# Optimization experiments

Measured on AMD Instinct MI355X. Metric: run time of the kernel, lower is better.

Reference implementation:

```python
import jax, jax.numpy as jnp
import numpy as np

NUM_EXPERTS = 8
HIDDEN = 1024
INTERMEDIATE = 2816
TOTAL_TOKENS = 4096  # 512 tokens per expert


def setup_inputs() -> dict:
    key = jax.random.key(0)
    k_x, k1, k2, k3 = jax.random.split(key, 4)
    hiddens = jax.random.normal(k_x, (TOTAL_TOKENS, HIDDEN), dtype=jnp.float32)
    # tokens assumed pre-sorted by expert; equal-sized groups here
    batch_sizes = jnp.full((NUM_EXPERTS,), TOTAL_TOKENS // NUM_EXPERTS, dtype=jnp.int64)
    w1_weight = jax.random.normal(k1, (NUM_EXPERTS, HIDDEN, INTERMEDIATE), dtype=jnp.float32)
    w2_weight = jax.random.normal(k2, (NUM_EXPERTS, INTERMEDIATE, HIDDEN), dtype=jnp.float32)
    w3_weight = jax.random.normal(k3, (NUM_EXPERTS, HIDDEN, INTERMEDIATE), dtype=jnp.float32)
    return {
        "hiddens": hiddens,
        "w1_weight": w1_weight,
        "w2_weight": w2_weight,
        "w3_weight": w3_weight,
        "batch_sizes": batch_sizes,
    }


def _grouped_moe(hiddens, w1, w2, w3, batch_sizes):
    """Grouped SwiGLU FFN: tokens are contiguous per expert (sizes = batch_sizes).

    Jit-safe formulation: map each token to its expert id, then run one masked
    dense GEMM trio per expert (small fixed expert count). Zero rows contribute
    exactly zero (silu(0)*0 == 0), so no final masking of the output is needed.
    """
    num_experts = w1.shape[0]
    total_tokens = hiddens.shape[0]
    bounds = jnp.cumsum(batch_sizes)  # [E] exclusive-right boundaries
    expert_ids = jnp.searchsorted(bounds, jnp.arange(total_tokens), side="right")  # [T]
    out = jnp.zeros((total_tokens, w2.shape[-1]), dtype=hiddens.dtype)
    for e in range(num_experts):
        mask = (expert_ids == e)[:, None]  # [T, 1]
        xe = jnp.where(mask, hiddens, 0)   # zero out other experts' tokens
        up = jax.nn.silu(xe @ w1[e]) * (xe @ w3[e])  # [T, F] SwiGLU
        out = out + up @ w2[e]             # [T, H]
    return out


def reference(hiddens, w1_weight, w2_weight, w3_weight, batch_sizes):
    return _grouped_moe(hiddens, w1_weight, w2_weight, w3_weight, batch_sizes)
```

## Files before the change

kernel.cpp:

```cpp
#include <hip/hip_runtime.h>
#include <hip/hip_bf16.h>

#define NE 8
#define HD 1024
#define ID 2816
#define TT 4096
#define BM 128
#define BK 32
#define BN1 64
#define BN2 64
#define MAXMT (TT / BM + NE)
#define NKS1 (HD / BK)
#define NKS2 (ID / BK)
#define ATILE 8192

typedef __attribute__((ext_vector_type(4))) float f32x4;
typedef __attribute__((ext_vector_type(8))) short s16x8;
typedef __attribute__((ext_vector_type(4))) int i32x4;

__device__ __forceinline__ unsigned int f2bfpk(float lo, float hi) {
  float2 t; t.x = lo; t.y = hi;
  union { __hip_bfloat162 h2; unsigned int u; } cv;
  cv.h2 = __float22bfloat162_rn(t);
  return cv.u;
}

__device__ __forceinline__ void lds_barrier() {
  asm volatile("s_waitcnt lgkmcnt(0)" ::: "memory");
  __builtin_amdgcn_s_barrier();
}

__device__ __forceinline__ void glds16(const void* g, void* l) {
  __builtin_amdgcn_global_load_lds(
      (const __attribute__((address_space(1))) void*)g,
      (__attribute__((address_space(3))) void*)l, 16, 0, 0);
}

__device__ __forceinline__ bool map_tile(const void* bsp, int mt, int& e,
                                         int& mstart, int& rowend) {
  const int* w = (const int*)bsp;
  bool is64 = (w[1] == 0) && (w[3] == 0) && (w[5] == 0) && (w[7] == 0) &&
              ((w[0] | w[2] | w[4] | w[6]) != 0);
  long long start = 0;
  int rem = mt;
  for (int i = 0; i < NE; ++i) {
    long long b = is64 ? ((const long long*)bsp)[i] : (long long)w[i];
    if (b < 0) b = 0;
    int tiles = (int)((b + BM - 1) / BM);
    if (rem < tiles) {
      long long m0 = start + (long long)rem * BM;
      long long me = start + b;
      if (m0 >= TT) return false;
      if (me > TT) me = TT;
      e = i; mstart = (int)m0; rowend = (int)me;
      return true;
    }
    rem -= tiles;
    start += b;
  }
  return false;
}

__global__ __launch_bounds__(256) void cvt_xt(const float* __restrict__ x,
                                              const void* __restrict__ bsp,
                                              unsigned short* __restrict__ xt) {
  int mt = blockIdx.x >> 5;
  int ks = blockIdx.x & 31;
  int e, mstart, rowend;
  if (!map_tile(bsp, mt, e, mstart, rowend)) return;
  int t = threadIdx.x;
  int lane = t & 63;
  int r = lane & 15, q = lane >> 4;
  unsigned short* ob = xt + ((size_t)mt * NKS1 + ks) * (ATILE / 2);
#pragma unroll
  for (int h = 0; h < 2; ++h) {
    int f = h * 4 + (t >> 6);
    int row = mstart + f * 16 + r;
    s16x8 o = (s16x8)0;
    if (row < rowend) {
      const float* src = x + (size_t)row * HD + ks * 32 + q * 8;
      f32x4 v0 = *(const f32x4*)src;
      f32x4 v1 = *(const f32x4*)(src + 4);
      unsigned int d0 = f2bfpk(v0[0], v0[1]), d1 = f2bfpk(v0[2], v0[3]);
      unsigned int d2 = f2bfpk(v1[0], v1[1]), d3 = f2bfpk(v1[2], v1[3]);
      o[0] = (short)d0; o[1] = (short)(d0 >> 16);
      o[2] = (short)d1; o[3] = (short)(d1 >> 16);
      o[4] = (short)d2; o[5] = (short)(d2 >> 16);
      o[6] = (short)d3; o[7] = (short)(d3 >> 16);
    }
    *(s16x8*)(ob + h * 2048 + t * 8) = o;
  }
}

__global__ __launch_bounds__(256, 3) void moe_gemm1(
    const unsigned short* __restrict__ xt, const float* __restrict__ w1,
    const float* __restrict__ w3, const void* __restrict__ bsp,
    __hip_bfloat16* __restrict__ up) {
  __shared__ __align__(16) char As[4][ATILE];
  __shared__ __align__(16) char B1s[2][4096];
  __shared__ __align__(16) char B3s[2][4096];

  const int NWG = (ID / BN1) * MAXMT;
  int bid = blockIdx.x;
  int logical = (bid & 7) * (NWG >> 3) + (bid >> 3);
  int mt = logical % MAXMT;
  int nt = logical / MAXMT;
  int e, mstart, rowend;
  if (!map_tile(bsp, mt, e, mstart, rowend)) return;
  const int n0 = nt * BN1;
  const int tid = threadIdx.x;
  const int lane = tid & 63;
  const int wv = tid >> 6;
  const int wr = wv >> 1, wc = wv & 1;
  const int q = lane >> 4, r16 = lane & 15;

  const int b_n = tid & 63, b_kq = tid >> 6;
  const int boff = (b_n >> 4) * 1024 + b_kq * 256 + (b_n & 15) * 16;
  const char* agp = (const char*)xt + (size_t)mt * NKS1 * ATILE + tid * 16;
  const float* w1c = w1 + (size_t)e * HD * ID + (size_t)(8 * b_kq) * ID + n0 + b_n;
  const float* w3c = w3 + (size_t)e * HD * ID + (size_t)(8 * b_kq) * ID + n0 + b_n;

  f32x4 acc1[4][2], acc3[4][2];
#pragma unroll
  for (int i = 0; i < 4; ++i)
#pragma unroll
    for (int j = 0; j < 2; ++j) { acc1[i][j] = (f32x4)0.f; acc3[i][j] = (f32x4)0.f; }

  float Wa1[8], Wa3[8], Wb1[8], Wb3[8];

  auto gldsA = [&](int k, int buf) {
    const char* s = agp + (size_t)k * ATILE;
    char* d = &As[buf][0] + tid * 16;
    glds16(s, d);
    glds16(s + 4096, d + 4096);
  };
  auto loadB = [&](float* W1_, float* W3_) {
#pragma unroll
    for (int i = 0; i < 8; ++i) {
      W1_[i] = w1c[(size_t)i * ID];
      W3_[i] = w3c[(size_t)i * ID];
    }
    w1c += (size_t)BK * ID; w3c += (size_t)BK * ID;
  };
  auto storeB = [&](int buf, const float* W1_, const float* W3_) {
    i32x4 p1, p3;
    p1[0] = (int)f2bfpk(W1_[0], W1_[1]); p1[1] = (int)f2bfpk(W1_[2], W1_[3]);
    p1[2] = (int)f2bfpk(W1_[4], W1_[5]); p1[3] = (int)f2bfpk(W1_[6], W1_[7]);
    *(i32x4*)(B1s[buf] + boff) = p1;
    p3[0] = (int)f2bfpk(W3_[0], W3_[1]); p3[1] = (int)f2bfpk(W3_[2], W3_[3]);
    p3[2] = (int)f2bfpk(W3_[4], W3_[5]); p3[3] = (int)f2bfpk(W3_[6], W3_[7]);
    *(i32x4*)(B3s[buf] + boff) = p3;
  };
  auto compute = [&](int ab, int bb) {
    s16x8 a[4], b1[2], b3[2];
#pragma unroll
    for (int i = 0; i < 4; ++i)
      a[i] = *(const s16x8*)(As[ab] + (wr * 4 + i) * 1024 + lane * 16);
#pragma unroll
    for (int j = 0; j < 2; ++j) {
      b1[j] = *(const s16x8*)(B1s[bb] + (wc * 2 + j) * 1024 + lane * 16);
      b3[j] = *(const s16x8*)(B3s[bb] + (wc * 2 + j) * 1024 + lane * 16);
    }
#pragma unroll
    for (int i = 0; i < 4; ++i)
#pragma unroll
      for (int j = 0; j < 2; ++j) {
        acc1[i][j] = __builtin_amdgcn_mfma_f32_16x16x32_bf16(a[i], b1[j], acc1[i][j], 0, 0, 0);
        acc3[i][j] = __builtin_amdgcn_mfma_f32_16x16x32_bf16(a[i], b3[j], acc3[i][j], 0, 0, 0);
      }
  };

#define G1PHASE(AB, GD, BB, SB, LW1, LW3, SW1, SW3, KC)    \
  if (kt + (KC) + 2 < NKS1) {                              \
    gldsA(kt + (KC) + 2, (GD));                            \
    __builtin_amdgcn_sched_barrier(0);                     \
    loadB(LW1, LW3);                                       \
  }                                                        \
  compute((AB), (BB));                                     \
  if (kt + (KC) + 1 < NKS1) {                              \
    storeB((SB), SW1, SW3);                                \
    lds_barrier();                                         \
  }

  gldsA(0, 0); gldsA(1, 1);
  __builtin_amdgcn_sched_barrier(0);
  loadB(Wa1, Wa3);
  loadB(Wb1, Wb3);
  storeB(0, Wa1, Wa3);
  lds_barrier();

  for (int kt = 0; kt < NKS1; kt += 4) {
    G1PHASE(0, 2, 0, 1, Wa1, Wa3, Wb1, Wb3, 0)
    G1PHASE(1, 3, 1, 0, Wb1, Wb3, Wa1, Wa3, 1)
    G1PHASE(2, 0, 0, 1, Wa1, Wa3, Wb1, Wb3, 2)
    G1PHASE(3, 1, 1, 0, Wb1, Wb3, Wa1, Wa3, 3)
  }
#undef G1PHASE

#pragma unroll
  for (int i = 0; i < 4; ++i)
#pragma unroll
    for (int r = 0; r < 4; ++r) {
      int gm = mstart + wr * 64 + i * 16 + q * 4 + r;
      if (gm < rowend) {
#pragma unroll
        for (int j = 0; j < 2; ++j) {
          float v1 = acc1[i][j][r], v3 = acc3[i][j][r];
          float s = v1 / (1.f + __expf(-v1));
          up[(size_t)gm * ID + n0 + wc * 32 + j * 16 + r16] = __float2bfloat16(s * v3);
        }
      }
    }
}

__global__ __launch_bounds__(256, 3) void moe_gemm2(
    const __hip_bfloat16* __restrict__ up, const float* __restrict__ w2,
    const void* __restrict__ bsp, float* __restrict__ out) {
  __shared__ __align__(16) char As[2][BM * 80];
  __shared__ __align__(16) char Bs[2][4096];

  const int NWG = (HD / BN2) * MAXMT;
  int bid = blockIdx.x;
  int logical = (bid & 7) * (NWG >> 3) + (bid >> 3);
  int mt = logical % MAXMT;
  int nt = logical / MAXMT;
  int e, mstart, rowend;
  if (!map_tile(bsp, mt, e, mstart, rowend)) return;
  const int n0 = nt * BN2;
  const int tid = threadIdx.x;
  const int lane = tid & 63;
  const int wv = tid >> 6;
  const int wr = wv >> 1, wc = wv & 1;
  const int q = lane >> 4, r16 = lane & 15;

  const int a_k8 = (tid & 3) * 8;
  const int a_r0 = tid >> 2;
  const int b_n = tid & 63, b_kq = tid >> 6;
  const int boff = (b_n >> 4) * 1024 + b_kq * 256 + (b_n & 15) * 16;

  const bool ok0 = (mstart + a_r0) < rowend;
  const bool ok1 = (mstart + a_r0 + 64) < rowend;

  const __hip_bfloat16* uc = up + (size_t)(mstart + a_r0) * ID + a_k8;
  const float* w2c = w2 + (size_t)e * ID * HD + (size_t)(8 * b_kq) * HD + n0 + b_n;

  f32x4 acc[4][2];
#pragma unroll
  for (int i = 0; i < 4; ++i)
#pragma unroll
    for (int j = 0; j < 2; ++j) acc[i][j] = (f32x4)0.f;

  s16x8 Aa[2], Ab[2];
  float Wa[8], Wb[8];

  auto loadT = [&](s16x8* A, float* W_) {
    A[0] = ok0 ? *(const s16x8*)uc : (s16x8)0;
    A[1] = ok1 ? *(const s16x8*)(uc + (size_t)64 * ID) : (s16x8)0;
    uc += BK;
#pragma unroll
    for (int i = 0; i < 8; ++i) W_[i] = w2c[(size_t)i * HD];
    w2c += (size_t)BK * HD;
  };
  auto storeT = [&](int buf, const s16x8* A, const float* W_) {
    *(s16x8*)(As[buf] + a_r0 * 80 + a_k8 * 2) = A[0];
    *(s16x8*)(As[buf] + (a_r0 + 64) * 80 + a_k8 * 2) = A[1];
    i32x4 p;
    p[0] = (int)f2bfpk(W_[0], W_[1]); p[1] = (int)f2bfpk(W_[2], W_[3]);
    p[2] = (int)f2bfpk(W_[4], W_[5]); p[3] = (int)f2bfpk(W_[6], W_[7]);
    *(i32x4*)(Bs[buf] + boff) = p;
  };
  auto compute = [&](int buf) {
    s16x8 a[4], b[2];
#pragma unroll
    for (int i = 0; i < 4; ++i)
      a[i] = *(const s16x8*)(As[buf] + (wr * 64 + i * 16 + r16) * 80 + q * 16);
#pragma unroll
    for (int j = 0; j < 2; ++j)
      b[j] = *(const s16x8*)(Bs[buf] + (wc * 2 + j) * 1024 + lane * 16);
#pragma unroll
    for (int i = 0; i < 4; ++i)
#pragma unroll
      for (int j = 0; j < 2; ++j)
        acc[i][j] = __builtin_amdgcn_mfma_f32_16x16x32_bf16(a[i], b[j], acc[i][j], 0, 0, 0);
  };

#define G2PHASE(AB, SB, LA, LW, SA, SW, KC)                 \
  if (kt + (KC) + 2 < NKS2) { loadT(LA, LW); }              \
  compute(AB);                                              \
  if (kt + (KC) + 1 < NKS2) { storeT((SB), SA, SW); lds_barrier(); }

  loadT(Aa, Wa);
  loadT(Ab, Wb);
  storeT(0, Aa, Wa);
  lds_barrier();
  for (int kt = 0; kt < NKS2; kt += 2) {
    G2PHASE(0, 1, Aa, Wa, Ab, Wb, 0)
    G2PHASE(1, 0, Ab, Wb, Aa, Wa, 1)
  }
#undef G2PHASE

#pragma unroll
  for (int i = 0; i < 4; ++i)
#pragma unroll
    for (int r = 0; r < 4; ++r) {
      int gm = mstart + wr * 64 + i * 16 + q * 4 + r;
      if (gm < rowend) {
#pragma unroll
        for (int j = 0; j < 2; ++j)
          out[(size_t)gm * HD + n0 + wc * 32 + j * 16 + r16] = acc[i][j][r];
      }
    }
}

extern "C" void kernel_launch(void* const* d_in, const int* in_sizes, int n_in,
                              void* d_out, int out_size, void* d_ws, size_t ws_size,
                              hipStream_t stream) {
  const float* x = (const float*)d_in[0];
  const float* w1 = (const float*)d_in[1];
  const float* w2 = (const float*)d_in[2];
  const float* w3 = (const float*)d_in[3];
  const void* bs = d_in[4];
  float* out = (float*)d_out;
  unsigned short* xt = (unsigned short*)d_ws;
  __hip_bfloat16* up =
      (__hip_bfloat16*)((char*)d_ws + (size_t)MAXMT * NKS1 * ATILE);

  hipMemsetAsync(d_out, 0, (size_t)out_size * sizeof(float), stream);

  cvt_xt<<<dim3(MAXMT * NKS1), dim3(256), 0, stream>>>(x, bs, xt);
  moe_gemm1<<<dim3((ID / BN1) * MAXMT), dim3(256), 0, stream>>>(xt, w1, w3, bs, up);
  moe_gemm2<<<dim3((HD / BN2) * MAXMT), dim3(256), 0, stream>>>(up, w2, bs, out);
}
```

Baseline: 184.9 us.

## Load A operands straight from global into registers, bypassing LDS in both GEMMs

Both GEMMs now read the bf16 A operand straight from global memory into MFMA-fragment registers, and A tiles no longer pass through shared memory. The tiled X pre-layout kernel is replaced by a plain row-major fp32-to-bf16 conversion. The aim is to cut LDS traffic and LDS footprint, and gemm2 raises its occupancy hint from 3 to 4. In exchange, each lane issues 16-byte strided global loads across rows, which coalesce worse and rely on L2 hits. Rows past the group boundary read clamped addresses but are masked at store time.

```diff
diff --git a/kernel.cpp b/kernel.cpp
--- a/kernel.cpp
+++ b/kernel.cpp
@@ -12,7 +12,6 @@
 #define MAXMT (TT / BM + NE)
 #define NKS1 (HD / BK)
 #define NKS2 (ID / BK)
-#define ATILE 8192
 
 typedef __attribute__((ext_vector_type(4))) float f32x4;
 typedef __attribute__((ext_vector_type(8))) short s16x8;
@@ -28,12 +27,6 @@
 __device__ __forceinline__ void lds_barrier() {
   asm volatile("s_waitcnt lgkmcnt(0)" ::: "memory");
   __builtin_amdgcn_s_barrier();
-}
-
-__device__ __forceinline__ void glds16(const void* g, void* l) {
-  __builtin_amdgcn_global_load_lds(
-      (const __attribute__((address_space(1))) void*)g,
-      (__attribute__((address_space(3))) void*)l, 16, 0, 0);
 }
 
 __device__ __forceinline__ bool map_tile(const void* bsp, int mt, int& e,
@@ -61,42 +54,25 @@
   return false;
 }
 
-__global__ __launch_bounds__(256) void cvt_xt(const float* __restrict__ x,
-                                              const void* __restrict__ bsp,
-                                              unsigned short* __restrict__ xt) {
-  int mt = blockIdx.x >> 5;
-  int ks = blockIdx.x & 31;
-  int e, mstart, rowend;
-  if (!map_tile(bsp, mt, e, mstart, rowend)) return;
-  int t = threadIdx.x;
-  int lane = t & 63;
-  int r = lane & 15, q = lane >> 4;
-  unsigned short* ob = xt + ((size_t)mt * NKS1 + ks) * (ATILE / 2);
-#pragma unroll
-  for (int h = 0; h < 2; ++h) {
-    int f = h * 4 + (t >> 6);
-    int row = mstart + f * 16 + r;
-    s16x8 o = (s16x8)0;
-    if (row < rowend) {
-      const float* src = x + (size_t)row * HD + ks * 32 + q * 8;
-      f32x4 v0 = *(const f32x4*)src;
-      f32x4 v1 = *(const f32x4*)(src + 4);
-      unsigned int d0 = f2bfpk(v0[0], v0[1]), d1 = f2bfpk(v0[2], v0[3]);
-      unsigned int d2 = f2bfpk(v1[0], v1[1]), d3 = f2bfpk(v1[2], v1[3]);
-      o[0] = (short)d0; o[1] = (short)(d0 >> 16);
-      o[2] = (short)d1; o[3] = (short)(d1 >> 16);
-      o[4] = (short)d2; o[5] = (short)(d2 >> 16);
-      o[6] = (short)d3; o[7] = (short)(d3 >> 16);
-    }
-    *(s16x8*)(ob + h * 2048 + t * 8) = o;
-  }
+__global__ __launch_bounds__(256) void cvt_x(const float* __restrict__ x,
+                                             __hip_bfloat16* __restrict__ xb) {
+  size_t i = ((size_t)blockIdx.x * 256 + threadIdx.x) * 8;
+  f32x4 v0 = *(const f32x4*)(x + i);
+  f32x4 v1 = *(const f32x4*)(x + i + 4);
+  s16x8 o;
+  unsigned int p0 = f2bfpk(v0[0], v0[1]), p1 = f2bfpk(v0[2], v0[3]);
+  unsigned int p2 = f2bfpk(v1[0], v1[1]), p3 = f2bfpk(v1[2], v1[3]);
+  o[0] = (short)(p0 & 0xffff); o[1] = (short)(p0 >> 16);
+  o[2] = (short)(p1 & 0xffff); o[3] = (short)(p1 >> 16);
+  o[4] = (short)(p2 & 0xffff); o[5] = (short)(p2 >> 16);
+  o[6] = (short)(p3 & 0xffff); o[7] = (short)(p3 >> 16);
+  *(s16x8*)((unsigned short*)xb + i) = o;
 }
 
 __global__ __launch_bounds__(256, 3) void moe_gemm1(
-    const unsigned short* __restrict__ xt, const float* __restrict__ w1,
+    const __hip_bfloat16* __restrict__ xbf, const float* __restrict__ w1,
     const float* __restrict__ w3, const void* __restrict__ bsp,
     __hip_bfloat16* __restrict__ up) {
-  __shared__ __align__(16) char As[4][ATILE];
   __shared__ __align__(16) char B1s[2][4096];
   __shared__ __align__(16) char B3s[2][4096];
 
@@ -116,23 +92,42 @@
 
   const int b_n = tid & 63, b_kq = tid >> 6;
   const int boff = (b_n >> 4) * 1024 + b_kq * 256 + (b_n & 15) * 16;
-  const char* agp = (const char*)xt + (size_t)mt * NKS1 * ATILE + tid * 16;
   const float* w1c = w1 + (size_t)e * HD * ID + (size_t)(8 * b_kq) * ID + n0 + b_n;
   const float* w3c = w3 + (size_t)e * HD * ID + (size_t)(8 * b_kq) * ID + n0 + b_n;
 
+  const unsigned short* pA0;
+  const unsigned short* pA1;
+  const unsigned short* pA2;
+  const unsigned short* pA3;
+  {
+    const unsigned short* xb = (const unsigned short*)xbf;
+    int r0 = mstart + wr * 64 + r16;
+    int rowA[4];
+#pragma unroll
+    for (int i = 0; i < 4; ++i) {
+      int r = r0 + i * 16;
+      rowA[i] = r < TT ? r : TT - 1;
+    }
+    pA0 = xb + (size_t)rowA[0] * HD + q * 8;
+    pA1 = xb + (size_t)rowA[1] * HD + q * 8;
+    pA2 = xb + (size_t)rowA[2] * HD + q * 8;
+    pA3 = xb + (size_t)rowA[3] * HD + q * 8;
+  }
+
   f32x4 acc1[4][2], acc3[4][2];
 #pragma unroll
   for (int i = 0; i < 4; ++i)
 #pragma unroll
     for (int j = 0; j < 2; ++j) { acc1[i][j] = (f32x4)0.f; acc3[i][j] = (f32x4)0.f; }
 
+  s16x8 Aa[4], Ab[4];
   float Wa1[8], Wa3[8], Wb1[8], Wb3[8];
 
-  auto gldsA = [&](int k, int buf) {
-    const char* s = agp + (size_t)k * ATILE;
-    char* d = &As[buf][0] + tid * 16;
-    glds16(s, d);
-    glds16(s + 4096, d + 4096);
+  auto loadA = [&](s16x8* A, int k) {
+    A[0] = *(const s16x8*)(pA0 + k * BK);
+    A[1] = *(const s16x8*)(pA1 + k * BK);
+    A[2] = *(const s16x8*)(pA2 + k * BK);
+    A[3] = *(const s16x8*)(pA3 + k * BK);
   };
   auto loadB = [&](float* W1_, float* W3_) {
 #pragma unroll
@@ -151,11 +146,8 @@
     p3[2] = (int)f2bfpk(W3_[4], W3_[5]); p3[3] = (int)f2bfpk(W3_[6], W3_[7]);
     *(i32x4*)(B3s[buf] + boff) = p3;
   };
-  auto compute = [&](int ab, int bb) {
-    s16x8 a[4], b1[2], b3[2];
-#pragma unroll
-    for (int i = 0; i < 4; ++i)
-      a[i] = *(const s16x8*)(As[ab] + (wr * 4 + i) * 1024 + lane * 16);
+  auto compute = [&](const s16x8* A, int bb) {
+    s16x8 b1[2], b3[2];
 #pragma unroll
     for (int j = 0; j < 2; ++j) {
       b1[j] = *(const s16x8*)(B1s[bb] + (wc * 2 + j) * 1024 + lane * 16);
@@ -165,37 +157,26 @@
     for (int i = 0; i < 4; ++i)
 #pragma unroll
       for (int j = 0; j < 2; ++j) {
-        acc1[i][j] = __builtin_amdgcn_mfma_f32_16x16x32_bf16(a[i], b1[j], acc1[i][j], 0, 0, 0);
-        acc3[i][j] = __builtin_amdgcn_mfma_f32_16x16x32_bf16(a[i], b3[j], acc3[i][j], 0, 0, 0);
+        acc1[i][j] = __builtin_amdgcn_mfma_f32_16x16x32_bf16(A[i], b1[j], acc1[i][j], 0, 0, 0);
+        acc3[i][j] = __builtin_amdgcn_mfma_f32_16x16x32_bf16(A[i], b3[j], acc3[i][j], 0, 0, 0);
       }
   };
 
-#define G1PHASE(AB, GD, BB, SB, LW1, LW3, SW1, SW3, KC)    \
-  if (kt + (KC) + 2 < NKS1) {                              \
-    gldsA(kt + (KC) + 2, (GD));                            \
-    __builtin_amdgcn_sched_barrier(0);                     \
-    loadB(LW1, LW3);                                       \
-  }                                                        \
-  compute((AB), (BB));                                     \
-  if (kt + (KC) + 1 < NKS1) {                              \
-    storeB((SB), SW1, SW3);                                \
-    lds_barrier();                                         \
-  }
-
-  gldsA(0, 0); gldsA(1, 1);
-  __builtin_amdgcn_sched_barrier(0);
+  loadA(Aa, 0); loadA(Ab, 1);
   loadB(Wa1, Wa3);
   loadB(Wb1, Wb3);
   storeB(0, Wa1, Wa3);
   lds_barrier();
-
-  for (int kt = 0; kt < NKS1; kt += 4) {
-    G1PHASE(0, 2, 0, 1, Wa1, Wa3, Wb1, Wb3, 0)
-    G1PHASE(1, 3, 1, 0, Wb1, Wb3, Wa1, Wa3, 1)
-    G1PHASE(2, 0, 0, 1, Wa1, Wa3, Wb1, Wb3, 2)
-    G1PHASE(3, 1, 1, 0, Wb1, Wb3, Wa1, Wa3, 3)
-  }
-#undef G1PHASE
+  for (int kt = 0; kt < NKS1; kt += 2) {
+    if (kt + 2 < NKS1) loadB(Wa1, Wa3);
+    compute(Aa, 0);
+    if (kt + 2 < NKS1) loadA(Aa, kt + 2);
+    if (kt + 1 < NKS1) { storeB(1, Wb1, Wb3); lds_barrier(); }
+    if (kt + 3 < NKS1) loadB(Wb1, Wb3);
+    compute(Ab, 1);
+    if (kt + 3 < NKS1) loadA(Ab, kt + 3);
+    if (kt + 2 < NKS1) { storeB(0, Wa1, Wa3); lds_barrier(); }
+  }
 
 #pragma unroll
   for (int i = 0; i < 4; ++i)
@@ -213,10 +194,9 @@
     }
 }
 
-__global__ __launch_bounds__(256, 3) void moe_gemm2(
+__global__ __launch_bounds__(256, 4) void moe_gemm2(
     const __hip_bfloat16* __restrict__ up, const float* __restrict__ w2,
     const void* __restrict__ bsp, float* __restrict__ out) {
-  __shared__ __align__(16) char As[2][BM * 80];
   __shared__ __align__(16) char Bs[2][4096];
 
   const int NWG = (HD / BN2) * MAXMT;
@@ -233,71 +213,82 @@
   const int wr = wv >> 1, wc = wv & 1;
   const int q = lane >> 4, r16 = lane & 15;
 
-  const int a_k8 = (tid & 3) * 8;
-  const int a_r0 = tid >> 2;
   const int b_n = tid & 63, b_kq = tid >> 6;
   const int boff = (b_n >> 4) * 1024 + b_kq * 256 + (b_n & 15) * 16;
-
-  const bool ok0 = (mstart + a_r0) < rowend;
-  const bool ok1 = (mstart + a_r0 + 64) < rowend;
-
-  const __hip_bfloat16* uc = up + (size_t)(mstart + a_r0) * ID + a_k8;
   const float* w2c = w2 + (size_t)e * ID * HD + (size_t)(8 * b_kq) * HD + n0 + b_n;
 
+  const unsigned short* pA0;
+  const unsigned short* pA1;
+  const unsigned short* pA2;
+  const unsigned short* pA3;
+  {
+    const unsigned short* ub = (const unsigned short*)up;
+    int r0 = mstart + wr * 64 + r16;
+    int rowA[4];
+#pragma unroll
+    for (int i = 0; i < 4; ++i) {
+      int r = r0 + i * 16;
+      rowA[i] = r < TT ? r : TT - 1;
+    }
+    pA0 = ub + (size_t)rowA[0] * ID + q * 8;
+    pA1 = ub + (size_t)rowA[1] * ID + q * 8;
+    pA2 = ub + (size_t)rowA[2] * ID + q * 8;
+    pA3 = ub + (size_t)rowA[3] * ID + q * 8;
+  }
+
   f32x4 acc[4][2];
 #pragma unroll
   for (int i = 0; i < 4; ++i)
 #pragma unroll
     for (int j = 0; j < 2; ++j) acc[i][j] = (f32x4)0.f;
 
-  s16x8 Aa[2], Ab[2];
+  s16x8 Aa[4], Ab[4];
   float Wa[8], Wb[8];
 
-  auto loadT = [&](s16x8* A, float* W_) {
-    A[0] = ok0 ? *(const s16x8*)uc : (s16x8)0;
-    A[1] = ok1 ? *(const s16x8*)(uc + (size_t)64 * ID) : (s16x8)0;
-    uc += BK;
+  auto loadA = [&](s16x8* A, int k) {
+    A[0] = *(const s16x8*)(pA0 + k * BK);
+    A[1] = *(const s16x8*)(pA1 + k * BK);
+    A[2] = *(const s16x8*)(pA2 + k * BK);
+    A[3] = *(const s16x8*)(pA3 + k * BK);
+  };
+  auto loadB = [&](float* W_) {
 #pragma unroll
     for (int i = 0; i < 8; ++i) W_[i] = w2c[(size_t)i * HD];
     w2c += (size_t)BK * HD;
   };
-  auto storeT = [&](int buf, const s16x8* A, const float* W_) {
-    *(s16x8*)(As[buf] + a_r0 * 80 + a_k8 * 2) = A[0];
-    *(s16x8*)(As[buf] + (a_r0 + 64) * 80 + a_k8 * 2) = A[1];
+  auto storeB = [&](int buf, const float* W_) {
     i32x4 p;
     p[0] = (int)f2bfpk(W_[0], W_[1]); p[1] = (int)f2bfpk(W_[2], W_[3]);
     p[2] = (int)f2bfpk(W_[4], W_[5]); p[3] = (int)f2bfpk(W_[6], W_[7]);
     *(i32x4*)(Bs[buf] + boff) = p;
   };
-  auto compute = [&](int buf) {
-    s16x8 a[4], b[2];
+  auto compute = [&](const s16x8* A, int bb) {
+    s16x8 b[2];
+#pragma unroll
+    for (int j = 0; j < 2; ++j)
+      b[j] = *(const s16x8*)(Bs[bb] + (wc * 2 + j) * 1024 + lane * 16);
 #pragma unroll
     for (int i = 0; i < 4; ++i)
-      a[i] = *(const s16x8*)(As[buf] + (wr * 64 + i * 16 + r16) * 80 + q * 16);
-#pragma unroll
-    for (int j = 0; j < 2; ++j)
-      b[j] = *(const s16x8*)(Bs[buf] + (wc * 2 + j) * 1024 + lane * 16);
-#pragma unroll
-    for (int i = 0; i < 4; ++i)
 #pragma unroll
       for (int j = 0; j < 2; ++j)
-        acc[i][j] = __builtin_amdgcn_mfma_f32_16x16x32_bf16(a[i], b[j], acc[i][j], 0, 0, 0);
-  };
-
-#define G2PHASE(AB, SB, LA, LW, SA, SW, KC)                 \
-  if (kt + (KC) + 2 < NKS2) { loadT(LA, LW); }              \
-  compute(AB);                                              \
-  if (kt + (KC) + 1 < NKS2) { storeT((SB), SA, SW); lds_barrier(); }
-
-  loadT(Aa, Wa);
-  loadT(Ab, Wb);
-  storeT(0, Aa, Wa);
+        acc[i][j] = __builtin_amdgcn_mfma_f32_16x16x32_bf16(A[i], b[j], acc[i][j], 0, 0, 0);
+  };
+
+  loadA(Aa, 0); loadA(Ab, 1);
+  loadB(Wa);
+  loadB(Wb);
+  storeB(0, Wa);
   lds_barrier();
   for (int kt = 0; kt < NKS2; kt += 2) {
-    G2PHASE(0, 1, Aa, Wa, Ab, Wb, 0)
-    G2PHASE(1, 0, Ab, Wb, Aa, Wa, 1)
-  }
-#undef G2PHASE
+    if (kt + 2 < NKS2) loadB(Wa);
+    compute(Aa, 0);
+    if (kt + 2 < NKS2) loadA(Aa, kt + 2);
+    if (kt + 1 < NKS2) { storeB(1, Wb); lds_barrier(); }
+    if (kt + 3 < NKS2) loadB(Wb);
+    compute(Ab, 1);
+    if (kt + 3 < NKS2) loadA(Ab, kt + 3);
+    if (kt + 2 < NKS2) { storeB(0, Wa); lds_barrier(); }
+  }
 
 #pragma unroll
   for (int i = 0; i < 4; ++i)
@@ -321,13 +312,12 @@
   const float* w3 = (const float*)d_in[3];
   const void* bs = d_in[4];
   float* out = (float*)d_out;
-  unsigned short* xt = (unsigned short*)d_ws;
-  __hip_bfloat16* up =
-      (__hip_bfloat16*)((char*)d_ws + (size_t)MAXMT * NKS1 * ATILE);
+  __hip_bfloat16* xbf = (__hip_bfloat16*)d_ws;
+  __hip_bfloat16* up = (__hip_bfloat16*)((char*)d_ws + (size_t)TT * HD * 2);
 
   hipMemsetAsync(d_out, 0, (size_t)out_size * sizeof(float), stream);
 
-  cvt_xt<<<dim3(MAXMT * NKS1), dim3(256), 0, stream>>>(x, bs, xt);
-  moe_gemm1<<<dim3((ID / BN1) * MAXMT), dim3(256), 0, stream>>>(xt, w1, w3, bs, up);
+  cvt_x<<<dim3(TT * HD / (8 * 256)), dim3(256), 0, stream>>>(x, xbf);
+  moe_gemm1<<<dim3((ID / BN1) * MAXMT), dim3(256), 0, stream>>>(xbf, w1, w3, bs, up);
   moe_gemm2<<<dim3((HD / BN2) * MAXMT), dim3(256), 0, stream>>>(up, w2, bs, out);
 }
```

New measurement: 290.1 us. 1.57x slower.

## Shrink pipeline depth to raise occupancy and use direct-to-LDS loads in gemm2

Applied to the files above, without the earlier changes.

Both GEMM kernels now request 4 workgroups per CU instead of 3. The first GEMM's A-tile LDS ring drops from four buffers to two, and the register double-buffering of weights is cut to a single staging set. The second GEMM stops staging the bf16 intermediate through registers and loads it with global-to-LDS copies into an MFMA-fragment layout, clamping out-of-range rows instead of zeroing them. The aim is lower register and LDS pressure for more resident waves, at the cost of a shallower prefetch window that may expose global-load latency.

```diff
diff --git a/kernel.cpp b/kernel.cpp
--- a/kernel.cpp
+++ b/kernel.cpp
@@ -92,11 +92,11 @@
   }
 }
 
-__global__ __launch_bounds__(256, 3) void moe_gemm1(
+__global__ __launch_bounds__(256, 4) void moe_gemm1(
     const unsigned short* __restrict__ xt, const float* __restrict__ w1,
     const float* __restrict__ w3, const void* __restrict__ bsp,
     __hip_bfloat16* __restrict__ up) {
-  __shared__ __align__(16) char As[4][ATILE];
+  __shared__ __align__(16) char As[2][ATILE];
   __shared__ __align__(16) char B1s[2][4096];
   __shared__ __align__(16) char B3s[2][4096];
 
@@ -126,7 +126,7 @@
 #pragma unroll
     for (int j = 0; j < 2; ++j) { acc1[i][j] = (f32x4)0.f; acc3[i][j] = (f32x4)0.f; }
 
-  float Wa1[8], Wa3[8], Wb1[8], Wb3[8];
+  float Wc1[8], Wc3[8];
 
   auto gldsA = [&](int k, int buf) {
     const char* s = agp + (size_t)k * ATILE;
@@ -134,21 +134,21 @@
     glds16(s, d);
     glds16(s + 4096, d + 4096);
   };
-  auto loadB = [&](float* W1_, float* W3_) {
+  auto loadB = [&]() {
 #pragma unroll
     for (int i = 0; i < 8; ++i) {
-      W1_[i] = w1c[(size_t)i * ID];
-      W3_[i] = w3c[(size_t)i * ID];
+      Wc1[i] = w1c[(size_t)i * ID];
+      Wc3[i] = w3c[(size_t)i * ID];
     }
     w1c += (size_t)BK * ID; w3c += (size_t)BK * ID;
   };
-  auto storeB = [&](int buf, const float* W1_, const float* W3_) {
+  auto storeB = [&](int buf) {
     i32x4 p1, p3;
-    p1[0] = (int)f2bfpk(W1_[0], W1_[1]); p1[1] = (int)f2bfpk(W1_[2], W1_[3]);
-    p1[2] = (int)f2bfpk(W1_[4], W1_[5]); p1[3] = (int)f2bfpk(W1_[6], W1_[7]);
+    p1[0] = (int)f2bfpk(Wc1[0], Wc1[1]); p1[1] = (int)f2bfpk(Wc1[2], Wc1[3]);
+    p1[2] = (int)f2bfpk(Wc1[4], Wc1[5]); p1[3] = (int)f2bfpk(Wc1[6], Wc1[7]);
     *(i32x4*)(B1s[buf] + boff) = p1;
-    p3[0] = (int)f2bfpk(W3_[0], W3_[1]); p3[1] = (int)f2bfpk(W3_[2], W3_[3]);
-    p3[2] = (int)f2bfpk(W3_[4], W3_[5]); p3[3] = (int)f2bfpk(W3_[6], W3_[7]);
+    p3[0] = (int)f2bfpk(Wc3[0], Wc3[1]); p3[1] = (int)f2bfpk(Wc3[2], Wc3[3]);
+    p3[2] = (int)f2bfpk(Wc3[4], Wc3[5]); p3[3] = (int)f2bfpk(Wc3[6], Wc3[7]);
     *(i32x4*)(B3s[buf] + boff) = p3;
   };
   auto compute = [&](int ab, int bb) {
@@ -170,32 +170,29 @@
       }
   };
 
-#define G1PHASE(AB, GD, BB, SB, LW1, LW3, SW1, SW3, KC)    \
-  if (kt + (KC) + 2 < NKS1) {                              \
-    gldsA(kt + (KC) + 2, (GD));                            \
-    __builtin_amdgcn_sched_barrier(0);                     \
-    loadB(LW1, LW3);                                       \
-  }                                                        \
-  compute((AB), (BB));                                     \
-  if (kt + (KC) + 1 < NKS1) {                              \
-    storeB((SB), SW1, SW3);                                \
-    lds_barrier();                                         \
+  gldsA(0, 0);
+  __builtin_amdgcn_sched_barrier(0);
+  loadB();
+  storeB(0);
+  lds_barrier();
+  for (int kt = 0; kt < NKS1; kt += 2) {
+    if (kt + 1 < NKS1) {
+      gldsA(kt + 1, 1);
+      __builtin_amdgcn_sched_barrier(0);
+      loadB();
+      __builtin_amdgcn_sched_barrier(0);
+    }
+    compute(0, 0);
+    if (kt + 1 < NKS1) { storeB(1); lds_barrier(); }
+    if (kt + 2 < NKS1) {
+      gldsA(kt + 2, 0);
+      __builtin_amdgcn_sched_barrier(0);
+      loadB();
+      __builtin_amdgcn_sched_barrier(0);
+    }
+    compute(1, 1);
+    if (kt + 2 < NKS1) { storeB(0); lds_barrier(); }
   }
-
-  gldsA(0, 0); gldsA(1, 1);
-  __builtin_amdgcn_sched_barrier(0);
-  loadB(Wa1, Wa3);
-  loadB(Wb1, Wb3);
-  storeB(0, Wa1, Wa3);
-  lds_barrier();
-
-  for (int kt = 0; kt < NKS1; kt += 4) {
-    G1PHASE(0, 2, 0, 1, Wa1, Wa3, Wb1, Wb3, 0)
-    G1PHASE(1, 3, 1, 0, Wb1, Wb3, Wa1, Wa3, 1)
-    G1PHASE(2, 0, 0, 1, Wa1, Wa3, Wb1, Wb3, 2)
-    G1PHASE(3, 1, 1, 0, Wb1, Wb3, Wa1, Wa3, 3)
-  }
-#undef G1PHASE
 
 #pragma unroll
   for (int i = 0; i < 4; ++i)
@@ -213,10 +210,10 @@
     }
 }
 
-__global__ __launch_bounds__(256, 3) void moe_gemm2(
+__global__ __launch_bounds__(256, 4) void moe_gemm2(
     const __hip_bfloat16* __restrict__ up, const float* __restrict__ w2,
     const void* __restrict__ bsp, float* __restrict__ out) {
-  __shared__ __align__(16) char As[2][BM * 80];
+  __shared__ __align__(16) char As[2][ATILE];
   __shared__ __align__(16) char Bs[2][4096];
 
   const int NWG = (HD / BN2) * MAXMT;
@@ -233,50 +230,50 @@
   const int wr = wv >> 1, wc = wv & 1;
   const int q = lane >> 4, r16 = lane & 15;
 
-  const int a_k8 = (tid & 3) * 8;
-  const int a_r0 = tid >> 2;
   const int b_n = tid & 63, b_kq = tid >> 6;
   const int boff = (b_n >> 4) * 1024 + b_kq * 256 + (b_n & 15) * 16;
-
-  const bool ok0 = (mstart + a_r0) < rowend;
-  const bool ok1 = (mstart + a_r0 + 64) < rowend;
-
-  const __hip_bfloat16* uc = up + (size_t)(mstart + a_r0) * ID + a_k8;
   const float* w2c = w2 + (size_t)e * ID * HD + (size_t)(8 * b_kq) * HD + n0 + b_n;
 
+  int row0 = mstart + (tid >> 6) * 16 + (tid & 15);
+  int row1 = row0 + 64;
+  row0 = row0 < TT ? row0 : TT - 1;
+  row1 = row1 < TT ? row1 : TT - 1;
+  const char* uc0 = (const char*)up + ((size_t)row0 * ID + q * 8) * 2;
+  const char* uc1 = (const char*)up + ((size_t)row1 * ID + q * 8) * 2;
+
   f32x4 acc[4][2];
 #pragma unroll
   for (int i = 0; i < 4; ++i)
 #pragma unroll
     for (int j = 0; j < 2; ++j) acc[i][j] = (f32x4)0.f;
 
-  s16x8 Aa[2], Ab[2];
-  float Wa[8], Wb[8];
-
-  auto loadT = [&](s16x8* A, float* W_) {
-    A[0] = ok0 ? *(const s16x8*)uc : (s16x8)0;
-    A[1] = ok1 ? *(const s16x8*)(uc + (size_t)64 * ID) : (s16x8)0;
-    uc += BK;
-#pragma unroll
-    for (int i = 0; i < 8; ++i) W_[i] = w2c[(size_t)i * HD];
+  float Wc[8];
+
+  auto gldsA = [&](int buf) {
+    char* d = &As[buf][0] + tid * 16;
+    glds16(uc0, d);
+    glds16(uc1, d + 4096);
+    uc0 += BK * 2; uc1 += BK * 2;
+  };
+  auto loadB = [&]() {
+#pragma unroll
+    for (int i = 0; i < 8; ++i) Wc[i] = w2c[(size_t)i * HD];
     w2c += (size_t)BK * HD;
   };
-  auto storeT = [&](int buf, const s16x8* A, const float* W_) {
-    *(s16x8*)(As[buf] + a_r0 * 80 + a_k8 * 2) = A[0];
-    *(s16x8*)(As[buf] + (a_r0 + 64) * 80 + a_k8 * 2) = A[1];
+  auto storeB = [&](int buf) {
     i32x4 p;
-    p[0] = (int)f2bfpk(W_[0], W_[1]); p[1] = (int)f2bfpk(W_[2], W_[3]);
-    p[2] = (int)f2bfpk(W_[4], W_[5]); p[3] = (int)f2bfpk(W_[6], W_[7]);
+    p[0] = (int)f2bfpk(Wc[0], Wc[1]); p[1] = (int)f2bfpk(Wc[2], Wc[3]);
+    p[2] = (int)f2bfpk(Wc[4], Wc[5]); p[3] = (int)f2bfpk(Wc[6], Wc[7]);
     *(i32x4*)(Bs[buf] + boff) = p;
   };
-  auto compute = [&](int buf) {
+  auto compute = [&](int ab, int bb) {
     s16x8 a[4], b[2];
 #pragma unroll
     for (int i = 0; i < 4; ++i)
-      a[i] = *(const s16x8*)(As[buf] + (wr * 64 + i * 16 + r16) * 80 + q * 16);
+      a[i] = *(const s16x8*)(As[ab] + (wr * 4 + i) * 1024 + lane * 16);
 #pragma unroll
     for (int j = 0; j < 2; ++j)
-      b[j] = *(const s16x8*)(Bs[buf] + (wc * 2 + j) * 1024 + lane * 16);
+      b[j] = *(const s16x8*)(Bs[bb] + (wc * 2 + j) * 1024 + lane * 16);
 #pragma unroll
     for (int i = 0; i < 4; ++i)
 #pragma unroll
@@ -284,20 +281,29 @@
         acc[i][j] = __builtin_amdgcn_mfma_f32_16x16x32_bf16(a[i], b[j], acc[i][j], 0, 0, 0);
   };
 
-#define G2PHASE(AB, SB, LA, LW, SA, SW, KC)                 \
-  if (kt + (KC) + 2 < NKS2) { loadT(LA, LW); }              \
-  compute(AB);                                              \
-  if (kt + (KC) + 1 < NKS2) { storeT((SB), SA, SW); lds_barrier(); }
-
-  loadT(Aa, Wa);
-  loadT(Ab, Wb);
-  storeT(0, Aa, Wa);
+  gldsA(0);
+  __builtin_amdgcn_sched_barrier(0);
+  loadB();
+  storeB(0);
   lds_barrier();
   for (int kt = 0; kt < NKS2; kt += 2) {
-    G2PHASE(0, 1, Aa, Wa, Ab, Wb, 0)
-    G2PHASE(1, 0, Ab, Wb, Aa, Wa, 1)
+    if (kt + 1 < NKS2) {
+      gldsA(1);
+      __builtin_amdgcn_sched_barrier(0);
+      loadB();
+      __builtin_amdgcn_sched_barrier(0);
+    }
+    compute(0, 0);
+    if (kt + 1 < NKS2) { storeB(1); lds_barrier(); }
+    if (kt + 2 < NKS2) {
+      gldsA(0);
+      __builtin_amdgcn_sched_barrier(0);
+      loadB();
+      __builtin_amdgcn_sched_barrier(0);
+    }
+    compute(1, 1);
+    if (kt + 2 < NKS2) { storeB(0); lds_barrier(); }
   }
-#undef G2PHASE
 
 #pragma unroll
   for (int i = 0; i < 4; ++i)
```

After: 205.2 us. +11.0%, slower.
